# Optimization experiments

Hardware: AMD Instinct MI355X
Metric: run time of the kernel (lower is better)

Reference implementation:

```python
import jax, jax.numpy as jnp
import numpy as np

jax.config.update("jax_enable_x64", True)

B, S = 256, 256
TINY = float(np.finfo(np.float64).tiny)  # torch.finfo().tiny for double


def _matrix_tree_logZ(scores, mask):
    """scores: [B,S,S] float64, mask: [B,S] bool (col 0 is False).
    Returns sum over batch of log partition function (Matrix-Tree theorem)."""
    lens = mask.sum(-1)  # token counts per sentence (excludes root col)
    mask_r = mask.at[:, 0].set(True)  # index_fill(1, 0, 1)
    pair = mask_r[:, :, None] & mask_r[:, None, :]  # [B,S,S]
    s = jnp.where(pair, scores, -jnp.inf)
    m = jnp.max(s.reshape(s.shape[0], -1), axis=-1)  # [B] per-batch max for stability
    A = jnp.maximum(jnp.exp(s - m[:, None, None]), TINY)  # clamp like torch
    idx = jnp.arange(S)
    D = jnp.zeros_like(A).at[:, idx, idx].set(A.sum(-1))  # degree matrix
    eye = jnp.eye(S, dtype=A.dtype)
    # masked_scatter_: rows with mask_r True take (D - A) rows, else identity
    L = jnp.where(mask_r[:, :, None], D - A, eye)
    logZ = jnp.linalg.slogdet(L[:, 1:, 1:])[1] + m * lens
    return logZ.sum()


def setup_inputs() -> dict:
    key = jax.random.key(0)
    k1, k2 = jax.random.split(key)
    scores = jax.random.normal(k1, (B, S, S), dtype=jnp.float32)
    lens = jax.random.randint(k2, (B,), S // 2, S)  # sentence lengths
    pos = jnp.arange(S)
    # col 0 (pseudo root) False, padding beyond length False
    mask = (pos[None, :] >= 1) & (pos[None, :] < lens[:, None])
    return {"scores": scores, "mask": mask}


def reference(scores, mask):
    # mbr=True path: marginals = d logZ / d scores (computed in double like torch)
    s64 = scores.astype(jnp.float64)
    probs = jax.grad(_matrix_tree_logZ)(s64, mask)
    return probs.astype(jnp.float32)
```

## Files before the change

kernel.cpp:

```cpp
#include <hip/hip_runtime.h>
#include <math.h>


#define S 256
#define BB 256

__device__ __forceinline__ int rowmap(int lr, int kb) {
    int rt = lr >> 6;
    int rb = rt + (rt >= kb ? 1 : 0);
    return rb * 64 + (lr & 63);
}

__global__ __launch_bounds__(256) void k_max(const float* __restrict__ sc,
                                             float* __restrict__ partial) {
    int b = blockIdx.y, rg = blockIdx.x;
    const float4* p4 = (const float4*)(sc + (size_t)b * S * S + rg * 8192);
    int tid = threadIdx.x;
    float4 v[8];
    #pragma unroll
    for (int it = 0; it < 8; ++it) v[it] = p4[tid + 256 * it];
    float m = -1e30f;
    #pragma unroll
    for (int it = 0; it < 8; ++it)
        m = fmaxf(m, fmaxf(fmaxf(v[it].x, v[it].y), fmaxf(v[it].z, v[it].w)));
    for (int off = 32; off > 0; off >>= 1) m = fmaxf(m, __shfl_down(m, off));
    __shared__ float sm[4];
    if ((tid & 63) == 0) sm[tid >> 6] = m;
    __syncthreads();
    if (tid == 0) partial[b * 8 + rg] = fmaxf(fmaxf(sm[0], sm[1]), fmaxf(sm[2], sm[3]));
}

__global__ void k_n(const unsigned char* __restrict__ mk, const float* __restrict__ partial,
                    double* __restrict__ mb, int* __restrict__ nb) {
    int b = blockIdx.x, j = threadIdx.x;
    __shared__ int shc[4];

    const unsigned int* mw = (const unsigned int*)mk;
    unsigned int w0 = mw[0], w1 = mw[1];
    int mode = (w0 != 0u) ? 0 : ((w1 != 0u) ? 1 : 2);

    int c;
    if (mode == 0)      c = (mk[(size_t)b * S + j] != 0);
    else if (mode == 1) c = (((const int*)mk)[(size_t)b * S + j] != 0);
    else                c = (((const long long*)mk)[(size_t)b * S + j] != 0LL);

    int lane = j & 63, wid = j >> 6;
    int cs = c;
    for (int off = 32; off > 0; off >>= 1) cs += __shfl_down(cs, off);
    if (lane == 0) shc[wid] = cs;
    __syncthreads();
    if (j == 0) {
        nb[b] = shc[0] + shc[1] + shc[2] + shc[3];
        float mm = partial[b * 8];
        #pragma unroll
        for (int q = 1; q < 8; ++q) mm = fmaxf(mm, partial[b * 8 + q]);
        mb[b] = (double)mm;
    }
}

__global__ __launch_bounds__(256) void k_build(const float* __restrict__ sc,
                                               const double* __restrict__ mb,
                                               const int* __restrict__ nb,
                                               double* __restrict__ Mg) {
    int b = blockIdx.y;
    int wid = threadIdx.x >> 6, lane = threadIdx.x & 63;
    int p = blockIdx.x * 4 + wid;
    int n = nb[b];
    double m = mb[b];
    __shared__ double se[4][260];
    double* Mrow = Mg + ((size_t)b * S + p) * S;
    bool act = (p < n);
    double ssum = 0.0;
    #pragma unroll
    for (int c4 = 0; c4 < 4; ++c4) {
        int j = lane + 64 * c4;
        double ev = 0.0;
        if (act && j <= n)
            ev = (double)expf((float)((double)sc[((size_t)b * S + (p + 1)) * S + j] - m));
        se[wid][j] = ev;
        ssum += ev;
    }
    for (int off = 32; off > 0; off >>= 1) ssum += __shfl_down(ssum, off);
    ssum = __shfl(ssum, 0);
    __syncthreads();
    #pragma unroll
    for (int c4 = 0; c4 < 4; ++c4) {
        int j = lane + 64 * c4;
        double v;
        if (act && j < n) v = ((j == p) ? ssum : 0.0) - se[wid][j + 1];
        else              v = (j == p) ? 1.0 : 0.0;
        Mrow[j] = v;
    }
}

__global__ __launch_bounds__(256) void k_gjrow(double* __restrict__ Mg, double* __restrict__ Pg,
                                               int kb) {
    int b = blockIdx.x, tid = threadIdx.x;
    double* M = Mg + (size_t)b * S * S;
    double* P = Pg + (size_t)b * 4096;
    __shared__ double PT[64][66];
    __shared__ double Rs[64][200];
    __shared__ double rbuf[2][64];
    __shared__ double cbuf[2][64];

    int i = tid >> 2, g = tid & 3, c0 = g << 4;
    double c[16];
    #pragma unroll
    for (int u = 0; u < 16; ++u)
        c[u] = M[(size_t)(kb * 64 + i) * S + kb * 64 + c0 + u];

    double rst[48];
    {
        int cidx = tid & 63;
        #pragma unroll
        for (int rep = 0; rep < 16; ++rep) {
            int r = rep * 4 + (tid >> 6);
            #pragma unroll
            for (int cc = 0; cc < 3; ++cc) {
                int j = cc * 64 + cidx;
                rst[rep * 3 + cc] = M[(size_t)(kb * 64 + r) * S + rowmap(j, kb)];
            }
        }
    }

    if (i == 0) {
        #pragma unroll
        for (int u = 0; u < 16; ++u) rbuf[0][c0 + u] = c[u];
    }
    if (g == 0) cbuf[0][i] = c[0];

    for (int kt = 0; kt < 4; ++kt) {
        #pragma unroll
        for (int ks = 0; ks < 16; ++ks) {
            int k = kt * 16 + ks;
            const int par = ks & 1;
            __syncthreads();
            double pv = rbuf[par][k];
            double f  = cbuf[par][i];
            double rk[16];
            #pragma unroll
            for (int m2 = 0; m2 < 8; ++m2) {
                double2 t = *(const double2*)&rbuf[par][c0 + 2 * m2];
                rk[2 * m2] = t.x; rk[2 * m2 + 1] = t.y;
            }
            double pivinv = 1.0 / pv;
            if (i == k) {
                #pragma unroll
                for (int u = 0; u < 16; ++u)
                    c[u] = ((g == kt) && (u == ks)) ? pivinv : c[u] * pivinv;
            } else {
                double gm = f * pivinv;
                #pragma unroll
                for (int u = 0; u < 16; ++u)
                    c[u] = ((g == kt) && (u == ks)) ? (-gm) : fma(-gm, rk[u], c[u]);
            }
            if (i == k + 1) {
                #pragma unroll
                for (int u = 0; u < 16; ++u) rbuf[par ^ 1][c0 + u] = c[u];
            }
            if (ks < 15) { if (g == kt)     cbuf[par ^ 1][i] = c[ks + 1]; }
            else         { if (g == kt + 1) cbuf[par ^ 1][i] = c[0]; }
        }
    }
    #pragma unroll
    for (int u = 0; u < 16; ++u) {
        PT[c0 + u][i] = c[u];
        P[i * 64 + c0 + u] = c[u];
        M[(size_t)(kb * 64 + i) * S + kb * 64 + c0 + u] = c[u];
    }
    {
        int cidx = tid & 63;
        #pragma unroll
        for (int rep = 0; rep < 16; ++rep) {
            int r = rep * 4 + (tid >> 6);
            #pragma unroll
            for (int cc = 0; cc < 3; ++cc)
                Rs[r][cc * 64 + cidx] = rst[rep * 3 + cc];
        }
    }
    __syncthreads();

    int tx = tid & 15, ty = tid >> 4;
    double2 acc[4][6];
    #pragma unroll
    for (int q = 0; q < 4; ++q)
        #pragma unroll
        for (int w = 0; w < 6; ++w) acc[q][w] = double2{0.0, 0.0};

    for (int s = 0; s < 64; ++s) {
        double2 p01 = *(const double2*)&PT[s][4 * ty];
        double2 p23 = *(const double2*)&PT[s][4 * ty + 2];
        #pragma unroll
        for (int w = 0; w < 6; ++w) {
            double2 r = *(const double2*)&Rs[s][2 * tx + 32 * w];
            acc[0][w].x = fma(p01.x, r.x, acc[0][w].x); acc[0][w].y = fma(p01.x, r.y, acc[0][w].y);
            acc[1][w].x = fma(p01.y, r.x, acc[1][w].x); acc[1][w].y = fma(p01.y, r.y, acc[1][w].y);
            acc[2][w].x = fma(p23.x, r.x, acc[2][w].x); acc[2][w].y = fma(p23.x, r.y, acc[2][w].y);
            acc[3][w].x = fma(p23.y, r.x, acc[3][w].x); acc[3][w].y = fma(p23.y, r.y, acc[3][w].y);
        }
    }
    #pragma unroll
    for (int q = 0; q < 4; ++q) {
        size_t row = (size_t)(kb * 64 + 4 * ty + q) * S;
        #pragma unroll
        for (int w = 0; w < 6; ++w) {
            int j = 2 * tx + 32 * w;
            *(double2*)&M[row + rowmap(j, kb)] = acc[q][w];
        }
    }
}

__global__ __launch_bounds__(512) void k_upd(double* __restrict__ Mg, int kb) {
    int b = blockIdx.x;
    double* M = Mg + (size_t)b * S * S;
    int tid = threadIdx.x;
    __shared__ double Hs[16][258];
    __shared__ double FTs[16][98];
    int tx = tid & 31, ty = tid >> 5;

    for (int half = 0; half < 2; ++half) {
        double2 acc[6][4];
        #pragma unroll
        for (int q = 0; q < 6; ++q)
            #pragma unroll
            for (int w = 0; w < 4; ++w) acc[q][w] = double2{0.0, 0.0};

        for (int ck = 0; ck < 4; ++ck) {
            __syncthreads();
            #pragma unroll
            for (int rep = 0; rep < 8; ++rep) {
                int idx = rep * 512 + tid;
                int kk = idx >> 8, col = idx & 255;
                Hs[kk][col] = M[(size_t)(kb * 64 + ck * 16 + kk) * S + col];
            }
            #pragma unroll
            for (int rep = 0; rep < 3; ++rep) {
                int idx = rep * 512 + tid;
                int kk = idx & 15, lr = idx >> 4;
                FTs[kk][lr] = M[(size_t)rowmap(half * 96 + lr, kb) * S + kb * 64 + ck * 16 + kk];
            }
            __syncthreads();
            for (int kk = 0; kk < 16; ++kk) {
                double2 f01 = *(const double2*)&FTs[kk][6 * ty];
                double2 f23 = *(const double2*)&FTs[kk][6 * ty + 2];
                double2 f45 = *(const double2*)&FTs[kk][6 * ty + 4];
                #pragma unroll
                for (int w = 0; w < 4; ++w) {
                    double2 h = *(const double2*)&Hs[kk][2 * tx + 64 * w];
                    acc[0][w].x = fma(f01.x, h.x, acc[0][w].x); acc[0][w].y = fma(f01.x, h.y, acc[0][w].y);
                    acc[1][w].x = fma(f01.y, h.x, acc[1][w].x); acc[1][w].y = fma(f01.y, h.y, acc[1][w].y);
                    acc[2][w].x = fma(f23.x, h.x, acc[2][w].x); acc[2][w].y = fma(f23.x, h.y, acc[2][w].y);
                    acc[3][w].x = fma(f23.y, h.x, acc[3][w].x); acc[3][w].y = fma(f23.y, h.y, acc[3][w].y);
                    acc[4][w].x = fma(f45.x, h.x, acc[4][w].x); acc[4][w].y = fma(f45.x, h.y, acc[4][w].y);
                    acc[5][w].x = fma(f45.y, h.x, acc[5][w].x); acc[5][w].y = fma(f45.y, h.y, acc[5][w].y);
                }
            }
        }
        #pragma unroll
        for (int q = 0; q < 6; ++q) {
            size_t row = (size_t)rowmap(half * 96 + ty * 6 + q, kb) * S;
            #pragma unroll
            for (int w = 0; w < 4; ++w) {
                int j0 = 2 * tx + 64 * w;
                if (w == kb) {
                    *(double2*)&M[row + j0] = double2{-acc[q][w].x, -acc[q][w].y};
                } else {
                    double2 old = *(const double2*)&M[row + j0];
                    *(double2*)&M[row + j0] = double2{old.x - acc[q][w].x, old.y - acc[q][w].y};
                }
            }
        }
    }
}

__global__ __launch_bounds__(256) void k_xt(const double* __restrict__ Mg,
                                            float* __restrict__ outF,
                                            double* __restrict__ Dg) {
    int b = blockIdx.y, t = blockIdx.x;
    int r = t & 3, c = t >> 2;
    const double* M = Mg + (size_t)b * S * S;
    __shared__ float L[64][65];
    int tid = threadIdx.x;
    int cc = tid & 63;
    #pragma unroll
    for (int rep = 0; rep < 16; ++rep) {
        int rr = rep * 4 + (tid >> 6);
        L[rr][cc] = (float)M[(size_t)(64 * r + rr) * S + 64 * c + cc];
    }
    if (r == c && tid < 64)
        Dg[(size_t)b * S + 64 * r + tid] = M[(size_t)(64 * r + tid) * S + 64 * r + tid];
    __syncthreads();
    int pp = tid & 63;
    #pragma unroll
    for (int rep = 0; rep < 16; ++rep) {
        int qq = rep * 4 + (tid >> 6);
        int orow = 64 * c + qq + 1, ocol = 64 * r + pp + 1;
        if (orow < 256 && ocol < 256)
            outF[((size_t)b * S + orow) * S + ocol] = L[pp][qq];
    }
}

__global__ __launch_bounds__(256) void k_epi2(const float* __restrict__ sc,
                                              const double* __restrict__ Dg,
                                              const double* __restrict__ mb,
                                              const int* __restrict__ nb,
                                              float* __restrict__ out) {
    int b = blockIdx.y;
    int idx4 = blockIdx.x * 256 + threadIdx.x;
    int i = idx4 >> 6;
    int jq = idx4 & 63;
    int n = nb[b];
    float m = (float)mb[b];
    size_t base = ((size_t)b * S + i) * S + 4 * jq;
    float4 xf = *(const float4*)(out + base);
    float4 s4 = *(const float4*)(sc + base);
    double dg = (i >= 1) ? Dg[(size_t)b * S + i - 1] : 0.0;
    float xfa[4] = {xf.x, xf.y, xf.z, xf.w};
    float sa[4]  = {s4.x, s4.y, s4.z, s4.w};
    float ra[4];
    #pragma unroll
    for (int comp = 0; comp < 4; ++comp) {
        int j = 4 * jq + comp;
        float v = 0.0f;
        if (i >= 1 && i <= n && j <= n) {
            double A = (double)expf(sa[comp] - m);
            double sub = (j >= 1) ? (double)xfa[comp] : 0.0;
            v = (float)(A * (dg - sub));
        }
        ra[comp] = v;
    }
    *(float4*)(out + base) = float4{ra[0], ra[1], ra[2], ra[3]};
}

extern "C" void kernel_launch(void* const* d_in, const int* in_sizes, int n_in,
                              void* d_out, int out_size, void* d_ws, size_t ws_size,
                              hipStream_t stream) {
    (void)in_sizes; (void)n_in; (void)out_size; (void)ws_size;
    const float* sc = (const float*)d_in[0];
    const unsigned char* mk = (const unsigned char*)d_in[1];
    double* ws = (double*)d_ws;

    double* M  = ws;
    double* P  = M + (size_t)BB * S * S;
    double* mb = P + (size_t)BB * 4096;
    int*    nb = (int*)(mb + BB);
    double* Dg = mb + 2 * BB;
    float*  partial = (float*)P;
    float*  out = (float*)d_out;

    k_max<<<dim3(8, BB), 256, 0, stream>>>(sc, partial);
    k_n<<<BB, 256, 0, stream>>>(mk, partial, mb, nb);
    k_build<<<dim3(64, BB), 256, 0, stream>>>(sc, mb, nb, M);
    for (int kb = 0; kb < 4; ++kb) {
        k_gjrow<<<BB, 256, 0, stream>>>(M, P, kb);
        k_upd<<<BB, 512, 0, stream>>>(M, kb);
    }
    k_xt<<<dim3(16, BB), 256, 0, stream>>>(M, out, Dg);
    k_epi2<<<dim3(64, BB), 256, 0, stream>>>(sc, Dg, mb, nb, out);
}
```

Measured before the change: 639.3 us.

## Fuse Gauss-Jordan pivot block and trailing update into one kernel per step

Merges k_gjrow and k_upd into a single k_step kernel that runs at 512 threads. The pivot-block inverse is computed in registers, and the transformed pivot row strip is kept in a 128KB shared buffer H, so the update phase reads it from LDS instead of reloading it from global memory. The P workspace and four kernel launches go away. The cost is that the large shared-memory footprint limits residency to one block per CU, and the pivot-row product is now staged in small chunks with more barriers.

```diff
diff --git a/kernel.cpp b/kernel.cpp
--- a/kernel.cpp
+++ b/kernel.cpp
@@ -93,131 +93,127 @@
     }
 }
 
-__global__ __launch_bounds__(256) void k_gjrow(double* __restrict__ Mg, double* __restrict__ Pg,
-                                               int kb) {
-    int b = blockIdx.x, tid = threadIdx.x;
-    double* M = Mg + (size_t)b * S * S;
-    double* P = Pg + (size_t)b * 4096;
-    __shared__ double PT[64][66];
-    __shared__ double Rs[64][200];
-    __shared__ double rbuf[2][64];
-    __shared__ double cbuf[2][64];
-
-    int i = tid >> 2, g = tid & 3, c0 = g << 4;
-    double c[16];
-    #pragma unroll
-    for (int u = 0; u < 16; ++u)
-        c[u] = M[(size_t)(kb * 64 + i) * S + kb * 64 + c0 + u];
-
-    double rst[48];
-    {
-        int cidx = tid & 63;
-        #pragma unroll
-        for (int rep = 0; rep < 16; ++rep) {
-            int r = rep * 4 + (tid >> 6);
-            #pragma unroll
-            for (int cc = 0; cc < 3; ++cc) {
-                int j = cc * 64 + cidx;
-                rst[rep * 3 + cc] = M[(size_t)(kb * 64 + r) * S + rowmap(j, kb)];
-            }
-        }
-    }
-
-    if (i == 0) {
-        #pragma unroll
-        for (int u = 0; u < 16; ++u) rbuf[0][c0 + u] = c[u];
-    }
-    if (g == 0) cbuf[0][i] = c[0];
-
-    for (int kt = 0; kt < 4; ++kt) {
-        #pragma unroll
-        for (int ks = 0; ks < 16; ++ks) {
-            int k = kt * 16 + ks;
-            const int par = ks & 1;
-            __syncthreads();
-            double pv = rbuf[par][k];
-            double f  = cbuf[par][i];
-            double rk[16];
-            #pragma unroll
-            for (int m2 = 0; m2 < 8; ++m2) {
-                double2 t = *(const double2*)&rbuf[par][c0 + 2 * m2];
-                rk[2 * m2] = t.x; rk[2 * m2 + 1] = t.y;
-            }
-            double pivinv = 1.0 / pv;
-            if (i == k) {
-                #pragma unroll
-                for (int u = 0; u < 16; ++u)
-                    c[u] = ((g == kt) && (u == ks)) ? pivinv : c[u] * pivinv;
-            } else {
-                double gm = f * pivinv;
-                #pragma unroll
-                for (int u = 0; u < 16; ++u)
-                    c[u] = ((g == kt) && (u == ks)) ? (-gm) : fma(-gm, rk[u], c[u]);
-            }
-            if (i == k + 1) {
-                #pragma unroll
-                for (int u = 0; u < 16; ++u) rbuf[par ^ 1][c0 + u] = c[u];
-            }
-            if (ks < 15) { if (g == kt)     cbuf[par ^ 1][i] = c[ks + 1]; }
-            else         { if (g == kt + 1) cbuf[par ^ 1][i] = c[0]; }
-        }
-    }
-    #pragma unroll
-    for (int u = 0; u < 16; ++u) {
-        PT[c0 + u][i] = c[u];
-        P[i * 64 + c0 + u] = c[u];
-        M[(size_t)(kb * 64 + i) * S + kb * 64 + c0 + u] = c[u];
-    }
-    {
-        int cidx = tid & 63;
-        #pragma unroll
-        for (int rep = 0; rep < 16; ++rep) {
-            int r = rep * 4 + (tid >> 6);
-            #pragma unroll
-            for (int cc = 0; cc < 3; ++cc)
-                Rs[r][cc * 64 + cidx] = rst[rep * 3 + cc];
-        }
-    }
-    __syncthreads();
-
-    int tx = tid & 15, ty = tid >> 4;
-    double2 acc[4][6];
-    #pragma unroll
-    for (int q = 0; q < 4; ++q)
-        #pragma unroll
-        for (int w = 0; w < 6; ++w) acc[q][w] = double2{0.0, 0.0};
-
-    for (int s = 0; s < 64; ++s) {
-        double2 p01 = *(const double2*)&PT[s][4 * ty];
-        double2 p23 = *(const double2*)&PT[s][4 * ty + 2];
-        #pragma unroll
-        for (int w = 0; w < 6; ++w) {
-            double2 r = *(const double2*)&Rs[s][2 * tx + 32 * w];
-            acc[0][w].x = fma(p01.x, r.x, acc[0][w].x); acc[0][w].y = fma(p01.x, r.y, acc[0][w].y);
-            acc[1][w].x = fma(p01.y, r.x, acc[1][w].x); acc[1][w].y = fma(p01.y, r.y, acc[1][w].y);
-            acc[2][w].x = fma(p23.x, r.x, acc[2][w].x); acc[2][w].y = fma(p23.x, r.y, acc[2][w].y);
-            acc[3][w].x = fma(p23.y, r.x, acc[3][w].x); acc[3][w].y = fma(p23.y, r.y, acc[3][w].y);
-        }
-    }
-    #pragma unroll
-    for (int q = 0; q < 4; ++q) {
-        size_t row = (size_t)(kb * 64 + 4 * ty + q) * S;
-        #pragma unroll
-        for (int w = 0; w < 6; ++w) {
-            int j = 2 * tx + 32 * w;
-            *(double2*)&M[row + rowmap(j, kb)] = acc[q][w];
-        }
-    }
-}
-
-__global__ __launch_bounds__(512) void k_upd(double* __restrict__ Mg, int kb) {
+__global__ __launch_bounds__(512) void k_step(double* __restrict__ Mg, int kb) {
     int b = blockIdx.x;
     double* M = Mg + (size_t)b * S * S;
     int tid = threadIdx.x;
-    __shared__ double Hs[16][258];
-    __shared__ double FTs[16][98];
+    __shared__ double H[64 * 256];
+    __shared__ double SCR[3104];
+
+    int i = tid >> 3, g = tid & 7, c0 = g << 3;
+    double c[8];
+    {
+        const double* src = M + (size_t)(kb * 64 + i) * S + kb * 64 + c0;
+        #pragma unroll
+        for (int m2 = 0; m2 < 4; ++m2) {
+            double2 t = *(const double2*)(src + 2 * m2);
+            c[2 * m2] = t.x; c[2 * m2 + 1] = t.y;
+        }
+    }
+    double* rbuf = SCR;
+    double* cbuf = SCR + 128;
+    if (i == 0) {
+        #pragma unroll
+        for (int u = 0; u < 8; ++u) rbuf[c0 + u] = c[u];
+    }
+    if (g == 0) cbuf[i] = c[0];
+    for (int k = 0; k < 64; ++k) {
+        int par = k & 1;
+        __syncthreads();
+        double pv = rbuf[par * 64 + k];
+        double f  = cbuf[par * 64 + i];
+        double rk[8];
+        #pragma unroll
+        for (int m2 = 0; m2 < 4; ++m2) {
+            double2 t = *(const double2*)&rbuf[par * 64 + c0 + 2 * m2];
+            rk[2 * m2] = t.x; rk[2 * m2 + 1] = t.y;
+        }
+        double pivinv = 1.0 / pv;
+        int kg = k >> 3, ks = k & 7;
+        if (i == k) {
+            #pragma unroll
+            for (int u = 0; u < 8; ++u)
+                c[u] = ((g == kg) && (u == ks)) ? pivinv : c[u] * pivinv;
+        } else {
+            double gm = f * pivinv;
+            #pragma unroll
+            for (int u = 0; u < 8; ++u)
+                c[u] = ((g == kg) && (u == ks)) ? (-gm) : fma(-gm, rk[u], c[u]);
+        }
+        int k1 = k + 1;
+        if (k1 < 64) {
+            if (i == k1) {
+                #pragma unroll
+                for (int u = 0; u < 8; ++u) rbuf[(par ^ 1) * 64 + c0 + u] = c[u];
+            }
+            if (g == (k1 >> 3)) cbuf[(par ^ 1) * 64 + i] = c[k1 & 7];
+        }
+    }
+    __syncthreads();
+
     int tx = tid & 31, ty = tid >> 5;
-
+    double* PT = SCR;
+    double* Rc = SCR + 512;
+    double2 ga[4][3];
+    #pragma unroll
+    for (int r = 0; r < 4; ++r)
+        #pragma unroll
+        for (int q = 0; q < 3; ++q) ga[r][q] = double2{0.0, 0.0};
+
+    for (int cs = 0; cs < 8; ++cs) {
+        if (g == cs) {
+            #pragma unroll
+            for (int u = 0; u < 8; ++u) PT[u * 64 + i] = c[u];
+        }
+        #pragma unroll
+        for (int rep = 0; rep < 3; ++rep) {
+            int idx = rep * 512 + tid;
+            int sL = idx / 192, jj = idx - sL * 192;
+            Rc[sL * 192 + jj] = M[(size_t)(kb * 64 + cs * 8 + sL) * S + rowmap(jj, kb)];
+        }
+        __syncthreads();
+        #pragma unroll
+        for (int sL = 0; sL < 8; ++sL) {
+            double2 p01 = *(const double2*)&PT[sL * 64 + 4 * ty];
+            double2 p23 = *(const double2*)&PT[sL * 64 + 4 * ty + 2];
+            double2 r0 = *(const double2*)&Rc[sL * 192 + 2 * tx];
+            double2 r1 = *(const double2*)&Rc[sL * 192 + 2 * tx + 64];
+            double2 r2 = *(const double2*)&Rc[sL * 192 + 2 * tx + 128];
+            ga[0][0].x = fma(p01.x, r0.x, ga[0][0].x); ga[0][0].y = fma(p01.x, r0.y, ga[0][0].y);
+            ga[0][1].x = fma(p01.x, r1.x, ga[0][1].x); ga[0][1].y = fma(p01.x, r1.y, ga[0][1].y);
+            ga[0][2].x = fma(p01.x, r2.x, ga[0][2].x); ga[0][2].y = fma(p01.x, r2.y, ga[0][2].y);
+            ga[1][0].x = fma(p01.y, r0.x, ga[1][0].x); ga[1][0].y = fma(p01.y, r0.y, ga[1][0].y);
+            ga[1][1].x = fma(p01.y, r1.x, ga[1][1].x); ga[1][1].y = fma(p01.y, r1.y, ga[1][1].y);
+            ga[1][2].x = fma(p01.y, r2.x, ga[1][2].x); ga[1][2].y = fma(p01.y, r2.y, ga[1][2].y);
+            ga[2][0].x = fma(p23.x, r0.x, ga[2][0].x); ga[2][0].y = fma(p23.x, r0.y, ga[2][0].y);
+            ga[2][1].x = fma(p23.x, r1.x, ga[2][1].x); ga[2][1].y = fma(p23.x, r1.y, ga[2][1].y);
+            ga[2][2].x = fma(p23.x, r2.x, ga[2][2].x); ga[2][2].y = fma(p23.x, r2.y, ga[2][2].y);
+            ga[3][0].x = fma(p23.y, r0.x, ga[3][0].x); ga[3][0].y = fma(p23.y, r0.y, ga[3][0].y);
+            ga[3][1].x = fma(p23.y, r1.x, ga[3][1].x); ga[3][1].y = fma(p23.y, r1.y, ga[3][1].y);
+            ga[3][2].x = fma(p23.y, r2.x, ga[3][2].x); ga[3][2].y = fma(p23.y, r2.y, ga[3][2].y);
+        }
+        __syncthreads();
+    }
+    #pragma unroll
+    for (int r = 0; r < 4; ++r)
+        #pragma unroll
+        for (int q = 0; q < 3; ++q) {
+            int col = rowmap(2 * tx + 64 * q, kb);
+            *(double2*)&H[(4 * ty + r) * 256 + col] = ga[r][q];
+        }
+    #pragma unroll
+    for (int u = 0; u < 8; ++u) H[i * 256 + kb * 64 + c0 + u] = c[u];
+    __syncthreads();
+
+    #pragma unroll
+    for (int rep = 0; rep < 16; ++rep) {
+        int idx = rep * 512 + tid;
+        int row = idx >> 7, col2 = idx & 127;
+        *(double2*)&M[(size_t)(kb * 64 + row) * S + 2 * col2] =
+            *(const double2*)&H[row * 256 + 2 * col2];
+    }
+
+    double* FT = SCR;
     for (int half = 0; half < 2; ++half) {
         double2 acc[6][4];
         #pragma unroll
@@ -227,26 +223,22 @@
 
         for (int ck = 0; ck < 4; ++ck) {
             __syncthreads();
-            #pragma unroll
-            for (int rep = 0; rep < 8; ++rep) {
-                int idx = rep * 512 + tid;
-                int kk = idx >> 8, col = idx & 255;
-                Hs[kk][col] = M[(size_t)(kb * 64 + ck * 16 + kk) * S + col];
-            }
             #pragma unroll
             for (int rep = 0; rep < 3; ++rep) {
                 int idx = rep * 512 + tid;
                 int kk = idx & 15, lr = idx >> 4;
-                FTs[kk][lr] = M[(size_t)rowmap(half * 96 + lr, kb) * S + kb * 64 + ck * 16 + kk];
+                FT[kk * 194 + lr] =
+                    M[(size_t)rowmap(half * 96 + lr, kb) * S + kb * 64 + ck * 16 + kk];
             }
             __syncthreads();
             for (int kk = 0; kk < 16; ++kk) {
-                double2 f01 = *(const double2*)&FTs[kk][6 * ty];
-                double2 f23 = *(const double2*)&FTs[kk][6 * ty + 2];
-                double2 f45 = *(const double2*)&FTs[kk][6 * ty + 4];
+                int kr = ck * 16 + kk;
+                double2 f01 = *(const double2*)&FT[kk * 194 + 6 * ty];
+                double2 f23 = *(const double2*)&FT[kk * 194 + 6 * ty + 2];
+                double2 f45 = *(const double2*)&FT[kk * 194 + 6 * ty + 4];
                 #pragma unroll
                 for (int w = 0; w < 4; ++w) {
-                    double2 h = *(const double2*)&Hs[kk][2 * tx + 64 * w];
+                    double2 h = *(const double2*)&H[kr * 256 + 2 * tx + 64 * w];
                     acc[0][w].x = fma(f01.x, h.x, acc[0][w].x); acc[0][w].y = fma(f01.x, h.y, acc[0][w].y);
                     acc[1][w].x = fma(f01.y, h.x, acc[1][w].x); acc[1][w].y = fma(f01.y, h.y, acc[1][w].y);
                     acc[2][w].x = fma(f23.x, h.x, acc[2][w].x); acc[2][w].y = fma(f23.x, h.y, acc[2][w].y);
@@ -258,7 +250,7 @@
         }
         #pragma unroll
         for (int q = 0; q < 6; ++q) {
-            size_t row = (size_t)rowmap(half * 96 + ty * 6 + q, kb) * S;
+            size_t row = (size_t)rowmap(half * 96 + 6 * ty + q, kb) * S;
             #pragma unroll
             for (int w = 0; w < 4; ++w) {
                 int j0 = 2 * tx + 64 * w;
@@ -341,20 +333,17 @@
     double* ws = (double*)d_ws;
 
     double* M  = ws;
-    double* P  = M + (size_t)BB * S * S;
-    double* mb = P + (size_t)BB * 4096;
+    double* mb = M + (size_t)BB * S * S;
     int*    nb = (int*)(mb + BB);
     double* Dg = mb + 2 * BB;
-    float*  partial = (float*)P;
+    float*  partial = (float*)Dg;
     float*  out = (float*)d_out;
 
     k_max<<<dim3(8, BB), 256, 0, stream>>>(sc, partial);
     k_n<<<BB, 256, 0, stream>>>(mk, partial, mb, nb);
     k_build<<<dim3(64, BB), 256, 0, stream>>>(sc, mb, nb, M);
-    for (int kb = 0; kb < 4; ++kb) {
-        k_gjrow<<<BB, 256, 0, stream>>>(M, P, kb);
-        k_upd<<<BB, 512, 0, stream>>>(M, kb);
-    }
+    for (int kb = 0; kb < 4; ++kb)
+        k_step<<<BB, 512, 0, stream>>>(M, kb);
     k_xt<<<dim3(16, BB), 256, 0, stream>>>(M, out, Dg);
     k_epi2<<<dim3(64, BB), 256, 0, stream>>>(sc, Dg, mb, nb, out);
 }
```

After: 570.7 us. -10.7%, faster.
